# Kernel optimization log

Measured on AMD Instinct MI355X. Metric: run time of the kernel, lower is better.

Reference implementation:

```python
import jax, jax.numpy as jnp
import numpy as np

EPS = 1e-6


def _mp_cos_pointwise(p, q, M2):
    # p, q: [B, L, K]; M2: [C, K] (squared perspective weights)
    # cosine between (p*M_c) and (q*M_c) along K, per channel c -> [B, L, C]
    num = jnp.einsum('blk,blk,ck->blc', p, q, M2)
    pn = jnp.sqrt(jnp.maximum(jnp.einsum('blk,ck->blc', p * p, M2), EPS))
    qn = jnp.sqrt(jnp.maximum(jnp.einsum('blk,ck->blc', q * q, M2), EPS))
    return num / pn / qn


def setup_inputs() -> dict:
    key = jax.random.key(0)
    ks = jax.random.split(key, 10)
    B, Lq, Ld, K, C = 32, 200, 200, 200, 50
    f32 = jnp.float32
    def unif(k, shape):  # keras 'uniform' init: U(-0.05, 0.05)
        return jax.random.uniform(k, shape, f32, -0.05, 0.05)
    return {
        'q_rep': jax.random.normal(ks[0], (B, Lq, K), f32),
        'q_last': jax.random.normal(ks[1], (B, K), f32),
        'q_mask': jnp.ones((B, Lq), f32),
        'd_rep': jax.random.normal(ks[2], (B, Ld, K), f32),
        'd_last': jax.random.normal(ks[3], (B, K), f32),
        'd_mask': jnp.ones((B, Ld), f32),
        'full_M': unif(ks[4], (C, K)),
        'maxpool_M': unif(ks[5], (C, K)),
        'att_M': unif(ks[6], (C, K)),
        'max_att_M': unif(ks[7], (C, K)),
    }


def reference(q_rep, q_last, q_mask, d_rep, d_last, d_mask,
              full_M, maxpool_M, att_M, max_att_M):
    outputs = []

    # relevancy matrix: cosine(q[b,j,:], d[b,i,:]) -> [B, Ld, Lq]
    num = jnp.einsum('bik,bjk->bij', d_rep, q_rep)
    dn = jnp.sqrt(jnp.maximum(jnp.sum(d_rep * d_rep, -1), EPS))  # [B, Ld]
    qn = jnp.sqrt(jnp.maximum(jnp.sum(q_rep * q_rep, -1), EPS))  # [B, Lq]
    rel = num / qn[:, None, :] / dn[:, :, None]
    rel = rel * q_mask[:, None, :] * d_mask[:, :, None]

    # full matching: cosine(d[b,i]*M_c, q_last[b]*M_c) -> [B, Ld, C]
    M2 = full_M * full_M
    fnum = jnp.einsum('bik,bk,ck->bic', d_rep, q_last, M2)
    fpn = jnp.sqrt(jnp.maximum(jnp.einsum('bik,ck->bic', d_rep * d_rep, M2), EPS))
    fqn = jnp.sqrt(jnp.maximum(jnp.einsum('bk,ck->bc', q_last * q_last, M2), EPS))
    outputs.append(fnum / fpn / fqn[:, None, :])

    # maxpool matching: cosine(d[b,i]*M_c, q[b,j]*M_c) -> [B, Ld, Lq, C]
    M2 = maxpool_M * maxpool_M
    mnum = jnp.einsum('bik,bjk,ck->bijc', d_rep, q_rep, M2)
    mpn = jnp.sqrt(jnp.maximum(jnp.einsum('bik,ck->bic', d_rep * d_rep, M2), EPS))
    mqn = jnp.sqrt(jnp.maximum(jnp.einsum('bjk,ck->bjc', q_rep * q_rep, M2), EPS))
    mm = mnum / mpn[:, :, None, :] / mqn[:, None, :, :]
    outputs.append(jnp.concatenate([jnp.max(mm, axis=2), jnp.mean(mm, axis=2)], axis=2))

    # attentive matching: cosine-weighted q rep (no softmax -> normalize by sum)
    wq = jnp.einsum('bij,bjk->bik', rel, q_rep)
    wq = wq / (jnp.sum(rel, axis=-1) + EPS)[..., None]  # [B, Ld, K]
    outputs.append(_mp_cos_pointwise(d_rep, wq, att_M * att_M))

    # max-attentive matching: gather best-matching q word per d position
    idx = jnp.argmax(rel, axis=2)  # [B, Ld]
    max_q = jnp.take_along_axis(q_rep, idx[:, :, None], axis=1)  # [B, Ld, K]
    outputs.append(_mp_cos_pointwise(d_rep, max_q, max_att_M * max_att_M))

    return jnp.concatenate(outputs, axis=-1)  # [B, Ld, 5*C]
```

## Files before the change

kernel.cpp:

```cpp
#include <hip/hip_runtime.h>
#include <math.h>


#define EPS 1e-6f
#define NEG_HUGE -3.4e38f

typedef __bf16 bf16x8 __attribute__((ext_vector_type(8)));
typedef float f32x16 __attribute__((ext_vector_type(16)));

constexpr size_t OFF_M2ALL = 0;
constexpr size_t OFF_M2B16 = 40000;
constexpr size_t OFF_QB16  = 63296;
constexpr size_t OFF_DB16  = 915264;
constexpr size_t OFF_INVFPN= 1767232;
constexpr size_t OFF_INVMPN= 2087232;
constexpr size_t OFF_INVAPN= 2407232;
constexpr size_t OFF_INVXPN= 2727232;
constexpr size_t OFF_INVMQN= 3047232;
constexpr size_t OFF_INVXQN= 3367232;
constexpr size_t OFF_INVFQN= 3687232;
constexpr size_t OFF_INVDN = 3688832;
constexpr size_t OFF_INVQN = 3695232;
constexpr size_t OFF_IDX   = 3701632;
constexpr size_t OFF_WQ    = 3708032;
constexpr size_t OFF_G     = 4988032;
constexpr size_t OFF_PMAX2 = 6268032;
constexpr size_t OFF_PSUM2 = 6677632;

__global__ __launch_bounds__(256) void k_prep(
    const float* __restrict__ qR, const float* __restrict__ dR,
    const float* __restrict__ fM, const float* __restrict__ mM,
    const float* __restrict__ aM, const float* __restrict__ xM,
    unsigned short* __restrict__ qb16, unsigned short* __restrict__ db16,
    float* __restrict__ invdn, float* __restrict__ invqn,
    float* __restrict__ m2all, unsigned short* __restrict__ m2b16)
{
  int blk = blockIdx.x;
  int tid = threadIdx.x;
  if (blk < 4096) {
    int task = blk*4 + (tid >> 6);
    int l = tid & 63;
    int isQ = task >= 8192;
    int r = isQ ? task - 8192 : task;
    int b = r >> 8, j = r & 255;
    unsigned short* dst = (isQ ? qb16 : db16) + (size_t)r*208;
    if (j < 200) {
      const float* src = (isQ ? qR : dR) + (size_t)(b*200 + j)*200;
      float4 v = {0.f,0.f,0.f,0.f};
      if (l < 50) v = *(const float4*)(src + l*4);
      float s = fmaf(v.x,v.x, fmaf(v.y,v.y, fmaf(v.z,v.z, v.w*v.w)));
#pragma unroll
      for (int m = 32; m; m >>= 1) s += __shfl_xor(s, m);
      if (l == 0) {
        float rr = rsqrtf(fmaxf(s, EPS));
        if (isQ) invqn[b*200 + j] = rr; else invdn[b*200 + j] = rr;
      }
      if (l < 52) {
        ushort4 o = {0,0,0,0};
        if (l < 50) {
          __bf16 h0=(__bf16)v.x, h1=(__bf16)v.y, h2=(__bf16)v.z, h3=(__bf16)v.w;
          o.x = *(unsigned short*)&h0; o.y = *(unsigned short*)&h1;
          o.z = *(unsigned short*)&h2; o.w = *(unsigned short*)&h3;
        }
        *(ushort4*)(dst + l*4) = o;
      }
    } else {
      if (l < 52) { ushort4 z = {0,0,0,0}; *(ushort4*)(dst + l*4) = z; }
    }
  } else {
    int i = (blk - 4096)*256 + tid;
    if (i < 40000) {
      int m = i / 10000, r = i % 10000;
      const float* s = (m==0)?fM:(m==1)?mM:(m==2)?aM:xM;
      float v = s[r];
      m2all[i] = v*v;
    }
    if (i < 224*208) {
      int row = i / 208, k = i % 208;
      unsigned short o = 0;
      if (row < 200 && k < 200) {
        int m = row / 50, c = row % 50;
        const float* s = (m==0)?fM:(m==1)?mM:(m==2)?aM:xM;
        float v = s[c*200 + k];
        __bf16 h = (__bf16)(v*v);
        o = *(unsigned short*)&h;
      }
      m2b16[i] = o;
    }
  }
}

__global__ __launch_bounds__(256) void k_mid(
    const float* __restrict__ dR, const float* __restrict__ qR,
    const float* __restrict__ qL, const unsigned short* __restrict__ m2b16,
    float* __restrict__ invfpn, float* __restrict__ invmpn,
    float* __restrict__ invapn, float* __restrict__ invxpn,
    float* __restrict__ invmqn, float* __restrict__ invxqn,
    float* __restrict__ invfqn,
    const float* __restrict__ qMask, const float* __restrict__ dMask,
    const float* __restrict__ invdn, const float* __restrict__ invqn,
    float* __restrict__ wq, int* __restrict__ idxout)
{
  int tid = threadIdx.x;
  if (blockIdx.x < 702) {
    int w = tid >> 6, lane = tid & 63;
    int n = lane & 31, h = lane >> 5;
    int task = blockIdx.x*4 + w;
    if (task >= 2807) return;
    int rt = task / 7, nt = task % 7;
    int row = rt*32 + n;

    const float* src;
    if (row < 6400)       src = dR + (size_t)row*200;
    else if (row < 12800) src = qR + (size_t)(row-6400)*200;
    else                  src = qL + (size_t)(row-12800)*200;

    bf16x8 afrag[13];
#pragma unroll
    for (int ks = 0; ks < 13; ks++) {
      int ko = ks*16 + h*8;
      bf16x8 af;
      if (ko < 200) {
        float4 a0 = *(const float4*)(src + ko);
        float4 a1 = *(const float4*)(src + ko + 4);
        af[0] = (__bf16)(a0.x*a0.x); af[1] = (__bf16)(a0.y*a0.y);
        af[2] = (__bf16)(a0.z*a0.z); af[3] = (__bf16)(a0.w*a0.w);
        af[4] = (__bf16)(a1.x*a1.x); af[5] = (__bf16)(a1.y*a1.y);
        af[6] = (__bf16)(a1.z*a1.z); af[7] = (__bf16)(a1.w*a1.w);
      } else {
#pragma unroll
        for (int z = 0; z < 8; z++) af[z] = (__bf16)0.0f;
      }
      afrag[ks] = af;
    }

    f32x16 C;
#pragma unroll
    for (int z = 0; z < 16; z++) C[z] = 0.f;
    const unsigned short* bp = m2b16 + (size_t)(nt*32 + n)*208 + h*8;
#pragma unroll
    for (int ks = 0; ks < 13; ks++) {
      bf16x8 bf = *(const bf16x8*)(bp + ks*16);
      C = __builtin_amdgcn_mfma_f32_32x32x16_bf16(afrag[ks], bf, C, 0, 0, 0);
    }

    int cp = nt*32 + n;
    if (cp < 200) {
      int m = cp / 50, c = cp % 50;
#pragma unroll
      for (int r = 0; r < 16; r++) {
        int grow = rt*32 + (r & 3) + 8*(r >> 2) + 4*h;
        float v = rsqrtf(fmaxf(C[r], EPS));
        if (grow < 6400) {
          if (m == 0)      invfpn[grow*50 + c] = v;
          else if (m == 1) invmpn[grow*50 + c] = v;
          else if (m == 2) invapn[grow*50 + c] = v;
          else             invxpn[grow*50 + c] = v;
        } else if (grow < 12800) {
          int r2 = grow - 6400;
          if (m == 1)      invmqn[c*6400 + r2] = v;
          else if (m == 3) invxqn[r2*50 + c] = v;
        } else {
          if (m == 0)      invfqn[(grow-12800)*50 + c] = v;
        }
      }
    }
  } else {
    __shared__ float relsh[8][256];
    __shared__ float redv[4][8][2];
    __shared__ int   redi[4][8];
    __shared__ float invrs_sh[8];
    int blk = blockIdx.x - 702;
    int b  = blk / 25;
    int i0 = (blk % 25) * 8;
    int j = tid, jr = min(j, 199);
    bool jv = j < 200;
    const float* qb = qR + b*40000;
    const float* db = dR + (b*200 + i0)*200;
    float acc[8];
#pragma unroll
    for (int ii = 0; ii < 8; ii++) acc[ii] = 0.f;

    const float* qrow = qb + jr*200;
    for (int k4 = 0; k4 < 200; k4 += 4) {
      float4 qv = *(const float4*)(qrow + k4);
#pragma unroll
      for (int ii = 0; ii < 8; ii++) {
        acc[ii] = fmaf(db[ii*200 + k4 + 0], qv.x, acc[ii]);
        acc[ii] = fmaf(db[ii*200 + k4 + 1], qv.y, acc[ii]);
        acc[ii] = fmaf(db[ii*200 + k4 + 2], qv.z, acc[ii]);
        acc[ii] = fmaf(db[ii*200 + k4 + 3], qv.w, acc[ii]);
      }
    }

    float iqn = invqn[b*200 + jr];
    float qm  = qMask[b*200 + jr];
    int w = tid >> 6, l = tid & 63;
    float rv[8];
#pragma unroll
    for (int ii = 0; ii < 8; ii++) {
      float idn = invdn[b*200 + i0 + ii];
      float dm  = dMask[b*200 + i0 + ii];
      float r = acc[ii]*iqn*idn*qm*dm;
      rv[ii] = r;
      relsh[ii][j] = jv ? r : 0.f;
    }
#pragma unroll
    for (int ii = 0; ii < 8; ii++) {
      float vm = jv ? rv[ii] : NEG_HUGE;
      float vs = jv ? rv[ii] : 0.f;
      int bj = jr;
#pragma unroll
      for (int m = 32; m; m >>= 1) {
        float ov = __shfl_xor(vm, m);
        int   oj = __shfl_xor(bj, m);
        vs += __shfl_xor(vs, m);
        if (ov > vm || (ov == vm && oj < bj)) { vm = ov; bj = oj; }
      }
      if (l == 0) { redv[w][ii][0] = vm; redv[w][ii][1] = vs; redi[w][ii] = bj; }
    }
    __syncthreads();
    if (tid < 8) {
      float bv = redv[0][tid][0], ss = redv[0][tid][1]; int bj = redi[0][tid];
      for (int w2 = 1; w2 < 4; w2++) {
        ss += redv[w2][tid][1];
        float wv = redv[w2][tid][0]; int wj = redi[w2][tid];
        if (wv > bv || (wv == bv && wj < bj)) { bv = wv; bj = wj; }
      }
      invrs_sh[tid] = 1.f/(ss + EPS);
      idxout[b*200 + i0 + tid] = bj;
    }
    __syncthreads();

    int kl = min(tid, 199); bool kv = tid < 200;
    float acw[8];
#pragma unroll
    for (int ii = 0; ii < 8; ii++) acw[ii] = 0.f;
    for (int j0 = 0; j0 < 200; j0 += 4) {
      float qv0 = qb[(j0+0)*200 + kl];
      float qv1 = qb[(j0+1)*200 + kl];
      float qv2 = qb[(j0+2)*200 + kl];
      float qv3 = qb[(j0+3)*200 + kl];
#pragma unroll
      for (int ii = 0; ii < 8; ii++) {
        float4 rs = *(const float4*)&relsh[ii][j0];
        acw[ii] = fmaf(rs.x, qv0, acw[ii]);
        acw[ii] = fmaf(rs.y, qv1, acw[ii]);
        acw[ii] = fmaf(rs.z, qv2, acw[ii]);
        acw[ii] = fmaf(rs.w, qv3, acw[ii]);
      }
    }
#pragma unroll
    for (int ii = 0; ii < 8; ii++) {
      float v = acw[ii]*invrs_sh[ii];
      if (kv) wq[(size_t)(b*200 + i0 + ii)*200 + tid] = v;
    }
  }
}

__global__ __launch_bounds__(512,2) void k_big(
    const unsigned short* __restrict__ db16, const unsigned short* __restrict__ qb16,
    const float* __restrict__ m2all, const float* __restrict__ invmqn,
    float* __restrict__ pmax2, float* __restrict__ psum2,
    const float* __restrict__ dR, const float* __restrict__ qR,
    const float* __restrict__ qL, const float* __restrict__ wq,
    const int* __restrict__ idx, const unsigned short* __restrict__ m2b16,
    float* __restrict__ G)
{
  int tid = threadIdx.x;
  int w = tid >> 6, lane = tid & 63;
  int n = lane & 31, h = lane >> 5;
  if (blockIdx.x < 1600) {
    __shared__ __align__(16) unsigned short qsh[128*216];
    int b = blockIdx.x / 50, c = blockIdx.x % 50;
    const float* M2 = m2all + 10000 + c*200;
    const unsigned short* dbp = db16 + (size_t)(b*256 + w*32 + n)*208 + h*8;

    bf16x8 afrag[13];
#pragma unroll
    for (int ks = 0; ks < 13; ks++) afrag[ks] = *(const bf16x8*)(dbp + ks*16);

    float vm[16], vs[16];
#pragma unroll
    for (int r = 0; r < 16; r++) { vm[r] = NEG_HUGE; vs[r] = 0.f; }

    for (int jh = 0; jh < 2; jh++) {
      int nrows = jh ? 96 : 128;
      int njt   = jh ? 3 : 4;
      __syncthreads();
      {
        const unsigned short* src = qb16 + (size_t)(b*256 + jh*128)*208;
        const float* iqb = invmqn + c*6400 + b*200;
        for (int s = tid; s < nrows*26; s += 512) {
          int r = s / 26, ch = s - r*26;
          int j = jh*128 + r;
          float iq = (j < 200) ? iqb[j] : 0.f;
          int k0 = ch*8;
          bf16x8 v = *(const bf16x8*)(src + (size_t)r*208 + k0);
          float4 m0 = *(const float4*)(M2 + k0);
          float4 m1 = *(const float4*)(M2 + k0 + 4);
          bf16x8 o;
          o[0] = (__bf16)((float)v[0]*iq*m0.x); o[1] = (__bf16)((float)v[1]*iq*m0.y);
          o[2] = (__bf16)((float)v[2]*iq*m0.z); o[3] = (__bf16)((float)v[3]*iq*m0.w);
          o[4] = (__bf16)((float)v[4]*iq*m1.x); o[5] = (__bf16)((float)v[5]*iq*m1.y);
          o[6] = (__bf16)((float)v[6]*iq*m1.z); o[7] = (__bf16)((float)v[7]*iq*m1.w);
          *(bf16x8*)(qsh + r*216 + k0) = o;
        }
      }
      __syncthreads();

      for (int jt = 0; jt < njt; jt++) {
        f32x16 C;
#pragma unroll
        for (int z = 0; z < 16; z++) C[z] = 0.f;
        const unsigned short* bptr = qsh + (jt*32 + n)*216 + h*8;
#pragma unroll
        for (int ks = 0; ks < 13; ks++) {
          bf16x8 bf = *(const bf16x8*)(bptr + ks*16);
          C = __builtin_amdgcn_mfma_f32_32x32x16_bf16(afrag[ks], bf, C, 0, 0, 0);
        }
        bool jv = (jh*128 + jt*32 + n) < 200;
#pragma unroll
        for (int r = 0; r < 16; r++) {
          vm[r] = fmaxf(vm[r], jv ? C[r] : NEG_HUGE);
          vs[r] += C[r];
        }
      }
    }

#pragma unroll
    for (int r = 0; r < 16; r++) {
      float a = vm[r], s = vs[r];
#pragma unroll
      for (int m = 1; m <= 16; m <<= 1) {
        a = fmaxf(a, __shfl_xor(a, m));
        s += __shfl_xor(s, m);
      }
      vm[r] = a; vs[r] = s;
    }
    if (n == 0) {
#pragma unroll
      for (int r = 0; r < 16; r++) {
        int i = w*32 + (r & 3) + 8*(r >> 2) + 4*h;
        pmax2[(size_t)blockIdx.x*256 + i] = vm[r];
        psum2[(size_t)blockIdx.x*256 + i] = vs[r];
      }
    }
  } else {
    int task = (blockIdx.x - 1600)*8 + w;
    int mp = task / 400;
    int sub = task % 400;
    int rt = sub >> 1, nt = sub & 1;
    int row = rt*32 + n;
    int bb = row / 200;
    int msel = (mp == 0) ? 0 : (mp == 3) ? 3 : 2;

    const float* s0 = dR + (size_t)row*200;
    const float* s1;
    if (mp == 0)      s1 = qL + (size_t)bb*200;
    else if (mp == 1) s1 = wq + (size_t)row*200;
    else if (mp == 2) { s0 = wq + (size_t)row*200; s1 = s0; }
    else              s1 = qR + (size_t)(bb*200 + idx[row])*200;

    bf16x8 afrag[13];
#pragma unroll
    for (int ks = 0; ks < 13; ks++) {
      int ko = ks*16 + h*8;
      bf16x8 af;
      if (ko < 200) {
        float4 a0 = *(const float4*)(s0 + ko);
        float4 a1 = *(const float4*)(s0 + ko + 4);
        float4 b0 = *(const float4*)(s1 + ko);
        float4 b1 = *(const float4*)(s1 + ko + 4);
        af[0] = (__bf16)(a0.x*b0.x); af[1] = (__bf16)(a0.y*b0.y);
        af[2] = (__bf16)(a0.z*b0.z); af[3] = (__bf16)(a0.w*b0.w);
        af[4] = (__bf16)(a1.x*b1.x); af[5] = (__bf16)(a1.y*b1.y);
        af[6] = (__bf16)(a1.z*b1.z); af[7] = (__bf16)(a1.w*b1.w);
      } else {
#pragma unroll
        for (int z = 0; z < 8; z++) af[z] = (__bf16)0.0f;
      }
      afrag[ks] = af;
    }

    f32x16 C;
#pragma unroll
    for (int z = 0; z < 16; z++) C[z] = 0.f;
    const unsigned short* bp = m2b16 + (size_t)(msel*50 + nt*32 + n)*208 + h*8;
#pragma unroll
    for (int ks = 0; ks < 13; ks++) {
      bf16x8 bf = *(const bf16x8*)(bp + ks*16);
      C = __builtin_amdgcn_mfma_f32_32x32x16_bf16(afrag[ks], bf, C, 0, 0, 0);
    }
    int cc = nt*32 + n;
    if (cc < 50) {
#pragma unroll
      for (int r = 0; r < 16; r++) {
        int mrow = (r & 3) + 8*(r >> 2) + 4*h;
        G[(size_t)(mp*6400 + rt*32 + mrow)*50 + cc] = C[r];
      }
    }
  }
}

__global__ void k_out(
    const float* __restrict__ G, const float* __restrict__ pmax2,
    const float* __restrict__ psum2, const float* __restrict__ invfpn,
    const float* __restrict__ invmpn, const float* __restrict__ invapn,
    const float* __restrict__ invxpn, const float* __restrict__ invfqn,
    const float* __restrict__ invxqn, const int* __restrict__ idx,
    float* __restrict__ out)
{
  int row = blockIdx.x;
  int l = threadIdx.x;
  if (l >= 250) return;
  int b = row / 200, i = row % 200;
  int seg = l / 50, c = l % 50;
  float o;
  if (seg == 0) {
    o = G[(size_t)(0*6400 + row)*50 + c] * invfpn[row*50 + c] * invfqn[b*50 + c];
  } else if (seg == 1) {
    o = pmax2[(size_t)(b*50 + c)*256 + i] * invmpn[row*50 + c];
  } else if (seg == 2) {
    o = psum2[(size_t)(b*50 + c)*256 + i] * invmpn[row*50 + c] * (1.f/200.f);
  } else if (seg == 3) {
    o = G[(size_t)(1*6400 + row)*50 + c] * invapn[row*50 + c]
        * rsqrtf(fmaxf(G[(size_t)(2*6400 + row)*50 + c], EPS));
  } else {
    int jid = idx[row];
    o = G[(size_t)(3*6400 + row)*50 + c] * invxpn[row*50 + c]
        * invxqn[(b*200 + jid)*50 + c];
  }
  out[(size_t)row*250 + l] = o;
}

extern "C" void kernel_launch(void* const* d_in, const int* in_sizes, int n_in,
                              void* d_out, int out_size, void* d_ws, size_t ws_size,
                              hipStream_t stream) {
  const float* qR = (const float*)d_in[0];
  const float* qL = (const float*)d_in[1];
  const float* qM = (const float*)d_in[2];
  const float* dR = (const float*)d_in[3];
  const float* dM = (const float*)d_in[5];
  const float* fullM = (const float*)d_in[6];
  const float* mpM   = (const float*)d_in[7];
  const float* attM  = (const float*)d_in[8];
  const float* xM    = (const float*)d_in[9];

  float* ws  = (float*)d_ws;
  float* out = (float*)d_out;

  float* m2all  = ws + OFF_M2ALL;
  unsigned short* m2b16 = (unsigned short*)(ws + OFF_M2B16);
  unsigned short* qb16 = (unsigned short*)(ws + OFF_QB16);
  unsigned short* db16 = (unsigned short*)(ws + OFF_DB16);
  float* invfpn = ws + OFF_INVFPN;
  float* invmpn = ws + OFF_INVMPN;
  float* invapn = ws + OFF_INVAPN;
  float* invxpn = ws + OFF_INVXPN;
  float* invmqn = ws + OFF_INVMQN;
  float* invxqn = ws + OFF_INVXQN;
  float* invfqn = ws + OFF_INVFQN;
  float* invdn  = ws + OFF_INVDN;
  float* invqn  = ws + OFF_INVQN;
  int*   idxp   = (int*)(ws + OFF_IDX);
  float* wqp    = ws + OFF_WQ;
  float* G      = ws + OFF_G;
  float* pmax2  = ws + OFF_PMAX2;
  float* psum2  = ws + OFF_PSUM2;

  k_prep<<<4278, 256, 0, stream>>>(qR, dR, fullM, mpM, attM, xM,
                                   qb16, db16, invdn, invqn, m2all, m2b16);
  k_mid<<<1502, 256, 0, stream>>>(dR, qR, qL, m2b16,
                                  invfpn, invmpn, invapn, invxpn,
                                  invmqn, invxqn, invfqn,
                                  qM, dM, invdn, invqn, wqp, idxp);
  k_big<<<1800, 512, 0, stream>>>(db16, qb16, m2all, invmqn, pmax2, psum2,
                                  dR, qR, qL, wqp, idxp, m2b16, G);
  k_out<<<6400, 256, 0, stream>>>(G, pmax2, psum2, invfpn, invmpn, invapn,
                                  invxpn, invfqn, invxqn, idxp, out);
}
```

Baseline: 246.9 us.

## Reuse raw q tile across channels, apply M2 to d side and invmqn post-MFMA

The maxpool stage now stages each batch's raw bf16 q tile in shared memory once per block and reuses it across 5 channels, instead of rescaling q by M2 and invmqn in shared memory per (batch, channel) block. The M2 weight is folded into the d-side A fragments, built from fp32 d_rep, and the per-q inverse norm is applied to the accumulator after the MFMA. This cuts the grid for that stage from 1600 to 320 blocks and removes redundant q staging. In exchange, each warp runs a serial loop over 35 tiles, and the larger static shared array (224x216) may lower occupancy. The non-maxpool path also gets this larger allocation.

```diff
diff --git a/kernel.cpp b/kernel.cpp
--- a/kernel.cpp
+++ b/kernel.cpp
@@ -267,49 +267,56 @@
     const int* __restrict__ idx, const unsigned short* __restrict__ m2b16,
     float* __restrict__ G)
 {
+  __shared__ __align__(16) unsigned short qsh[224*216];
   int tid = threadIdx.x;
   int w = tid >> 6, lane = tid & 63;
   int n = lane & 31, h = lane >> 5;
-  if (blockIdx.x < 1600) {
-    __shared__ __align__(16) unsigned short qsh[128*216];
-    int b = blockIdx.x / 50, c = blockIdx.x % 50;
-    const float* M2 = m2all + 10000 + c*200;
-    const unsigned short* dbp = db16 + (size_t)(b*256 + w*32 + n)*208 + h*8;
-
-    bf16x8 afrag[13];
-#pragma unroll
-    for (int ks = 0; ks < 13; ks++) afrag[ks] = *(const bf16x8*)(dbp + ks*16);
-
-    float vm[16], vs[16];
-#pragma unroll
-    for (int r = 0; r < 16; r++) { vm[r] = NEG_HUGE; vs[r] = 0.f; }
-
-    for (int jh = 0; jh < 2; jh++) {
-      int nrows = jh ? 96 : 128;
-      int njt   = jh ? 3 : 4;
-      __syncthreads();
-      {
-        const unsigned short* src = qb16 + (size_t)(b*256 + jh*128)*208;
-        const float* iqb = invmqn + c*6400 + b*200;
-        for (int s = tid; s < nrows*26; s += 512) {
-          int r = s / 26, ch = s - r*26;
-          int j = jh*128 + r;
-          float iq = (j < 200) ? iqb[j] : 0.f;
-          int k0 = ch*8;
-          bf16x8 v = *(const bf16x8*)(src + (size_t)r*208 + k0);
-          float4 m0 = *(const float4*)(M2 + k0);
-          float4 m1 = *(const float4*)(M2 + k0 + 4);
-          bf16x8 o;
-          o[0] = (__bf16)((float)v[0]*iq*m0.x); o[1] = (__bf16)((float)v[1]*iq*m0.y);
-          o[2] = (__bf16)((float)v[2]*iq*m0.z); o[3] = (__bf16)((float)v[3]*iq*m0.w);
-          o[4] = (__bf16)((float)v[4]*iq*m1.x); o[5] = (__bf16)((float)v[5]*iq*m1.y);
-          o[6] = (__bf16)((float)v[6]*iq*m1.z); o[7] = (__bf16)((float)v[7]*iq*m1.w);
-          *(bf16x8*)(qsh + r*216 + k0) = o;
-        }
-      }
-      __syncthreads();
-
-      for (int jt = 0; jt < njt; jt++) {
+  if (blockIdx.x < 320) {
+    int b = blockIdx.x / 10, cg = blockIdx.x % 10;
+
+    {
+      const unsigned short* src = qb16 + (size_t)b*256*208;
+      for (int s = tid; s < 224*26; s += 512) {
+        int r = s / 26, ch = s - r*26;
+        *(bf16x8*)(qsh + r*216 + ch*8) =
+            *(const bf16x8*)(src + (size_t)r*208 + ch*8);
+      }
+    }
+    __syncthreads();
+
+    for (int t = w; t < 35; t += 8) {
+      int it = t % 7, c = cg*5 + t/7;
+      int drow = it*32 + n; if (drow > 199) drow = 199;
+      const float* dp  = dR + (size_t)(b*200 + drow)*200;
+      const float* m2p = m2all + 10000 + c*200;
+
+      bf16x8 afc[13];
+#pragma unroll
+      for (int ks = 0; ks < 13; ks++) {
+        int ko = ks*16 + h*8;
+        bf16x8 a;
+        if (ko < 200) {
+          float4 d0 = *(const float4*)(dp + ko);
+          float4 d1 = *(const float4*)(dp + ko + 4);
+          float4 m0 = *(const float4*)(m2p + ko);
+          float4 m1 = *(const float4*)(m2p + ko + 4);
+          a[0] = (__bf16)(d0.x*m0.x); a[1] = (__bf16)(d0.y*m0.y);
+          a[2] = (__bf16)(d0.z*m0.z); a[3] = (__bf16)(d0.w*m0.w);
+          a[4] = (__bf16)(d1.x*m1.x); a[5] = (__bf16)(d1.y*m1.y);
+          a[6] = (__bf16)(d1.z*m1.z); a[7] = (__bf16)(d1.w*m1.w);
+        } else {
+#pragma unroll
+          for (int z = 0; z < 8; z++) a[z] = (__bf16)0.0f;
+        }
+        afc[ks] = a;
+      }
+
+      float vm[16], vs[16];
+#pragma unroll
+      for (int r = 0; r < 16; r++) { vm[r] = NEG_HUGE; vs[r] = 0.f; }
+      const float* iqb = invmqn + (size_t)c*6400 + b*200;
+
+      for (int jt = 0; jt < 7; jt++) {
         f32x16 C;
 #pragma unroll
         for (int z = 0; z < 16; z++) C[z] = 0.f;
@@ -317,37 +324,41 @@
 #pragma unroll
         for (int ks = 0; ks < 13; ks++) {
           bf16x8 bf = *(const bf16x8*)(bptr + ks*16);
-          C = __builtin_amdgcn_mfma_f32_32x32x16_bf16(afrag[ks], bf, C, 0, 0, 0);
-        }
-        bool jv = (jh*128 + jt*32 + n) < 200;
+          C = __builtin_amdgcn_mfma_f32_32x32x16_bf16(afc[ks], bf, C, 0, 0, 0);
+        }
+        int j = jt*32 + n;
+        bool jvld = j < 200;
+        float iqj = jvld ? iqb[j] : 0.f;
 #pragma unroll
         for (int r = 0; r < 16; r++) {
-          vm[r] = fmaxf(vm[r], jv ? C[r] : NEG_HUGE);
-          vs[r] += C[r];
-        }
-      }
-    }
-
-#pragma unroll
-    for (int r = 0; r < 16; r++) {
-      float a = vm[r], s = vs[r];
-#pragma unroll
-      for (int m = 1; m <= 16; m <<= 1) {
-        a = fmaxf(a, __shfl_xor(a, m));
-        s += __shfl_xor(s, m);
-      }
-      vm[r] = a; vs[r] = s;
-    }
-    if (n == 0) {
+          float v = C[r]*iqj;
+          vs[r] += v;
+          vm[r] = fmaxf(vm[r], jvld ? v : NEG_HUGE);
+        }
+      }
+
 #pragma unroll
       for (int r = 0; r < 16; r++) {
-        int i = w*32 + (r & 3) + 8*(r >> 2) + 4*h;
-        pmax2[(size_t)blockIdx.x*256 + i] = vm[r];
-        psum2[(size_t)blockIdx.x*256 + i] = vs[r];
+        float a2 = vm[r], s2 = vs[r];
+#pragma unroll
+        for (int m = 1; m <= 16; m <<= 1) {
+          a2 = fmaxf(a2, __shfl_xor(a2, m));
+          s2 += __shfl_xor(s2, m);
+        }
+        vm[r] = a2; vs[r] = s2;
+      }
+      if (n == 0) {
+        size_t base = (size_t)(b*50 + c)*256;
+#pragma unroll
+        for (int r = 0; r < 16; r++) {
+          int i = it*32 + (r & 3) + 8*(r >> 2) + 4*h;
+          pmax2[base + i] = vm[r];
+          psum2[base + i] = vs[r];
+        }
       }
     }
   } else {
-    int task = (blockIdx.x - 1600)*8 + w;
+    int task = (blockIdx.x - 320)*8 + w;
     int mp = task / 400;
     int sub = task % 400;
     int rt = sub >> 1, nt = sub & 1;
@@ -475,8 +486,8 @@
                                   invfpn, invmpn, invapn, invxpn,
                                   invmqn, invxqn, invfqn,
                                   qM, dM, invdn, invqn, wqp, idxp);
-  k_big<<<1800, 512, 0, stream>>>(db16, qb16, m2all, invmqn, pmax2, psum2,
-                                  dR, qR, qL, wqp, idxp, m2b16, G);
+  k_big<<<520, 512, 0, stream>>>(db16, qb16, m2all, invmqn, pmax2, psum2,
+                                 dR, qR, qL, wqp, idxp, m2b16, G);
   k_out<<<6400, 256, 0, stream>>>(G, pmax2, psum2, invfpn, invmpn, invapn,
                                   invxpn, invfqn, invxqn, idxp, out);
 }
```

New measurement: 538.0 us. 118% more time.
